# Kernel tuning notes

Hardware: AMD Instinct MI355X
Metric: run time of the kernel (lower is better)

## Reference

```python
import jax, jax.numpy as jnp
import numpy as np

B, S, D, H = 2, 2048, 1024, 16
HD = D // H  # head_dim = 64
NEG = -1.0e9


def setup_inputs() -> dict:
    key = jax.random.key(0)
    ks = jax.random.split(key, 9)
    s = 1.0 / np.sqrt(D)
    return {
        "x": jax.random.normal(ks[0], (B, S, D), jnp.float32),
        "mask": jnp.ones((B, S), jnp.float32),
        "Wq": jax.random.normal(ks[1], (D, D), jnp.float32) * s,
        "bq": jnp.zeros((D,), jnp.float32),
        "Wk": jax.random.normal(ks[2], (D, D), jnp.float32) * s,
        "bk": jnp.zeros((D,), jnp.float32),
        "Wv": jax.random.normal(ks[3], (D, D), jnp.float32) * s,
        "bv": jnp.zeros((D,), jnp.float32),
        "Wo": jax.random.normal(ks[4], (D, D), jnp.float32) * s,
        "bo": jnp.zeros((D,), jnp.float32),
    }


def reference(x, mask, Wq, bq, Wk, bk, Wv, bv, Wo, bo):
    # QKV projections -> [B, H, S, HD]
    def proj(t, W, b):
        return (t @ W + b).reshape(B, S, H, HD).transpose(0, 2, 1, 3)

    q = proj(x, Wq, bq)
    k = proj(x, Wk, bk)
    v = proj(x, Wv, bv)

    scores = jnp.einsum("bhqd,bhkd->bhqk", q, k) / jnp.sqrt(jnp.asarray(HD, x.dtype))
    # causal mask: scores * m + (1-m) * -1e9 (matches original exactly)
    cm = jnp.tril(jnp.ones((S, S), x.dtype))[None, None]
    scores = scores * cm + (1.0 - cm) * NEG
    # 2D padding mask branch
    scores = scores + (1.0 - mask[:, None, None, :]) * NEG

    attn = jax.nn.softmax(scores, axis=-1)
    out = jnp.einsum("bhqk,bhkd->bqhd", attn, v).reshape(B, S, D)
    return out @ Wo + bo
```

## Files before the change

### kernel.cpp

```cpp
#include <hip/hip_runtime.h>
#include <hip/hip_bf16.h>
#include <cstdint>
#include <cstddef>

typedef __attribute__((ext_vector_type(8))) short short8;
typedef __attribute__((ext_vector_type(4))) float floatx4;
typedef __attribute__((ext_vector_type(2))) unsigned int uintx2;

#define MFMA16(a, b, c) __builtin_amdgcn_mfma_f32_16x16x32_bf16((a), (b), (c), 0, 0, 0)
#define LOG2E 1.44269504088896340736f
#define EXP2(x) __builtin_amdgcn_exp2f(x)

__device__ __forceinline__ unsigned short f2bf(float f) {
  unsigned int u = __builtin_bit_cast(unsigned int, f);
  u += 0x7fffu + ((u >> 16) & 1u);
  return (unsigned short)(u >> 16);
}

__device__ __forceinline__ unsigned int pk2(float a, float b) {
  float2 f; f.x = a; f.y = b;
  __hip_bfloat162 h = __float22bfloat162_rn(f);
  unsigned int u;
  __builtin_memcpy(&u, &h, 4);
  return u;
}

typedef __attribute__((address_space(1))) void gvoid_t;
typedef __attribute__((address_space(3))) void svoid_t;
__device__ __forceinline__ void gload_lds16(const void* g, void* l) {
  __builtin_amdgcn_global_load_lds((gvoid_t*)(uintptr_t)g, (svoid_t*)(uintptr_t)l, 16, 0, 0);
}

__global__ void convert_x(const float* __restrict__ x, unsigned short* __restrict__ xb) {
  int i = (blockIdx.x * 256 + threadIdx.x) * 4;
  floatx4 v = *(const floatx4*)(x + i);
  uintx2 o;
  o[0] = pk2(v[0], v[1]);
  o[1] = pk2(v[2], v[3]);
  *(uintx2*)(xb + i) = o;
}

__global__ void transpose_w(const float* __restrict__ Wq, const float* __restrict__ Wk,
                            const float* __restrict__ Wv, const float* __restrict__ Wo,
                            unsigned short* __restrict__ Wqkvt, unsigned short* __restrict__ Wot) {
  __shared__ float tile[32][33];
  int z = blockIdx.z;
  const float* W = (z == 0) ? Wq : (z == 1) ? Wk : (z == 2) ? Wv : Wo;
  unsigned short* out = (z == 3) ? Wot : (Wqkvt + (size_t)z * 1024 * 1024);
  int n0 = blockIdx.x * 32, k0 = blockIdx.y * 32;
  int tx = threadIdx.x, ty = threadIdx.y;
#pragma unroll
  for (int j = 0; j < 4; ++j)
    tile[ty + j * 8][tx] = W[(size_t)(k0 + ty + j * 8) * 1024 + n0 + tx];
  __syncthreads();
#pragma unroll
  for (int j = 0; j < 4; ++j)
    out[(size_t)(n0 + ty + j * 8) * 1024 + k0 + tx] = f2bf(tile[tx][ty + j * 8]);
}

#define GEMM_PROLOGUE()                                                        \
  __shared__ __align__(16) unsigned short As[128 * 64];                        \
  __shared__ __align__(16) unsigned short Bs[128 * 64];                        \
  const int tid = threadIdx.x;                                                 \
  const int lane = tid & 63;                                                   \
  const int wid = tid >> 6;                                                    \
  const int col = lane & 15;                                                   \
  const int quad = lane >> 4;                                                  \
  const int m0 = blockIdx.x * 128;                                             \
  const int n0 = blockIdx.y * 128;                                             \
  const int wm = wid >> 1;                                                     \
  const int wn = wid & 1;                                                      \
  floatx4 acc[4][4];                                                           \
  _Pragma("unroll") for (int i = 0; i < 4; ++i)                                \
      _Pragma("unroll") for (int j = 0; j < 4; ++j)                            \
          acc[i][j] = (floatx4)(0.f);                                          \
  _Pragma("unroll 1") for (int kt = 0; kt < 16; ++kt) {                        \
    __syncthreads();                                                           \
    _Pragma("unroll") for (int call = 0; call < 4; ++call) {                   \
      int c = call * 256 + tid;                                                \
      int r = c >> 3, ch = c & 7;                                              \
      gload_lds16(A + (size_t)(m0 + r) * 1024 + kt * 64 + ((ch ^ (r & 7)) * 8),\
                  As + (size_t)(call * 256 + wid * 64) * 8);                   \
      gload_lds16(Bt + (size_t)(n0 + r) * 1024 + kt * 64 + ((ch ^ (r & 7)) * 8),\
                  Bs + (size_t)(call * 256 + wid * 64) * 8);                   \
    }                                                                          \
    __syncthreads();                                                           \
    _Pragma("unroll") for (int ks = 0; ks < 2; ++ks) {                         \
      short8 af[4], bf[4];                                                     \
      _Pragma("unroll") for (int rt = 0; rt < 4; ++rt) {                       \
        int row = wm * 64 + rt * 16 + col;                                     \
        af[rt] = *(const short8*)&As[row * 64 + (((ks * 4 + quad) ^ (row & 7)) * 8)]; \
      }                                                                        \
      _Pragma("unroll") for (int ct = 0; ct < 4; ++ct) {                       \
        int row = wn * 64 + ct * 16 + col;                                     \
        bf[ct] = *(const short8*)&Bs[row * 64 + (((ks * 4 + quad) ^ (row & 7)) * 8)]; \
      }                                                                        \
      _Pragma("unroll") for (int rt = 0; rt < 4; ++rt)                         \
          _Pragma("unroll") for (int ct = 0; ct < 4; ++ct)                     \
              acc[rt][ct] = MFMA16(af[rt], bf[ct], acc[rt][ct]);               \
    }                                                                          \
  }

__global__ __launch_bounds__(256, 3)
void gemm_qkv(const unsigned short* __restrict__ A, const unsigned short* __restrict__ Bt,
              const float* __restrict__ bq, const float* __restrict__ bk,
              const float* __restrict__ bv,
              unsigned short* __restrict__ Qo, unsigned short* __restrict__ Ko,
              unsigned short* __restrict__ Vo) {
  GEMM_PROLOGUE()
  const int nseg = n0 >> 10;
  const float* bias = (nseg == 0) ? bq : ((nseg == 1) ? bk : bv);
#pragma unroll
  for (int rt = 0; rt < 4; ++rt) {
#pragma unroll
    for (int ct = 0; ct < 4; ++ct) {
      int mg = m0 + wm * 64 + rt * 16 + quad * 4;
      int ng = n0 + wn * 64 + ct * 16 + col;
      int c = ng & 1023;
      int hh = c >> 6, hd = c & 63;
      int b_ = mg >> 11, s = mg & 2047;
      float bb = bias[c];
      if (nseg == 2) {
        uintx2 pk;
        pk[0] = pk2(acc[rt][ct][0] + bb, acc[rt][ct][1] + bb);
        pk[1] = pk2(acc[rt][ct][2] + bb, acc[rt][ct][3] + bb);
        *(uintx2*)&Vo[(size_t)(b_ * 16 + hh) * 131072 + (size_t)hd * 2048 + s] = pk;
      } else {
        unsigned short* dst =
            ((nseg == 0) ? Qo : Ko) + ((size_t)(b_ * 16 + hh) * 2048 + s) * 64 + hd;
        float scl = (nseg == 0) ? (0.125f * LOG2E) : 1.0f;
#pragma unroll
        for (int i = 0; i < 4; ++i) dst[(size_t)i * 64] = f2bf((acc[rt][ct][i] + bb) * scl);
      }
    }
  }
}

__global__ __launch_bounds__(256, 3)
void gemm_out(const unsigned short* __restrict__ A, const unsigned short* __restrict__ Bt,
              const float* __restrict__ bo, float* __restrict__ Out) {
  GEMM_PROLOGUE()
#pragma unroll
  for (int rt = 0; rt < 4; ++rt) {
#pragma unroll
    for (int ct = 0; ct < 4; ++ct) {
      int mg = m0 + wm * 64 + rt * 16 + quad * 4;
      int ng = n0 + wn * 64 + ct * 16 + col;
      float bb = bo[ng];
#pragma unroll
      for (int i = 0; i < 4; ++i)
        Out[(size_t)(mg + i) * 1024 + ng] = acc[rt][ct][i] + bb;
    }
  }
}

__global__ __launch_bounds__(256, 4)
void flash_attn(const unsigned short* __restrict__ Q, const unsigned short* __restrict__ K,
                const unsigned short* __restrict__ Vt, const float* __restrict__ mask,
                unsigned short* __restrict__ O) {
  __shared__ __align__(16) unsigned short Ks[128 * 64];
  __shared__ __align__(16) unsigned short Vs[64 * 128];

  const int tid = threadIdx.x;
  const int lane = tid & 63;
  const int wid = tid >> 6;
  const int col = lane & 15;
  const int quad = lane >> 4;
  const int slot = (int)(blockIdx.x >> 8);
  const int g = (int)(blockIdx.x & 255);
  const int h8 = g >> 5;
  const int bh = g & 31;
  const int j = (slot == 0) ? (31 - h8) : (slot == 1) ? h8 : (slot == 2) ? (23 - h8) : (8 + h8);
  const int b = bh >> 4, h = bh & 15;
  const int q0 = j * 64;
  const int tdiag = j >> 1;

  const unsigned short* Qp = Q + (size_t)bh * 2048 * 64;
  const unsigned short* Kp = K + (size_t)bh * 2048 * 64;
  const unsigned short* Vp = Vt + (size_t)bh * 64 * 2048;
  const float* mp = mask + b * 2048;

  const int lr8 = lane >> 3, lc8 = lane & 7;
  const int lr16 = lane >> 4, lc16 = lane & 15;
  const floatx4 fzero = (floatx4)(0.f);
  const floatx4 fone = (floatx4)(1.f);

#pragma unroll
  for (int i = 0; i < 2; ++i) {
    int seg = wid * 2 + i;
    int r = seg * 8 + lr8;
    gload_lds16(Qp + (size_t)(q0 + r) * 64 + ((lc8 ^ (r & 7)) * 8), Ks + seg * 512);
  }
  __syncthreads();
  short8 qf[2];
  {
    int q = wid * 16 + col;
#pragma unroll
    for (int ks = 0; ks < 2; ++ks)
      qf[ks] = *(const short8*)&Ks[q * 64 + (((ks * 4 + quad) ^ (q & 7)) * 8)];
  }
  unsigned int mbits = 0;
  for (int t = 0; t <= tdiag; ++t) {
    float2 mv = *(const float2*)&mp[t * 128 + lane * 2];
    unsigned long long bb = __ballot(mv.x != 1.f || mv.y != 1.f);
    mbits |= (bb ? 1u : 0u) << t;
  }

  floatx4 o[4];
#pragma unroll
  for (int dt = 0; dt < 4; ++dt) o[dt] = fzero;
  float mrow = -1e30f;
  float lrow = 0.f;

#pragma unroll 1
  for (int t = 0; t <= tdiag; ++t) {
    __syncthreads();
#pragma unroll
    for (int i = 0; i < 4; ++i) {
      int seg = wid * 4 + i;
      int r = seg * 8 + lr8;
      gload_lds16(Kp + (size_t)(t * 128 + r) * 64 + ((lc8 ^ (r & 7)) * 8), Ks + seg * 512);
    }
#pragma unroll
    for (int i = 0; i < 4; ++i) {
      int seg = wid * 4 + i;
      int r = seg * 4 + lr16;
      gload_lds16(Vp + (size_t)r * 2048 + t * 128 + ((lc16 ^ (r & 15)) * 8), Vs + seg * 512);
    }
    __syncthreads();

    floatx4 sc[8];
    __builtin_amdgcn_s_setprio(1);
#pragma unroll
    for (int rt = 0; rt < 8; ++rt) {
      int kr = rt * 16 + col;
      short8 kf0 = *(const short8*)&Ks[kr * 64 + ((quad ^ (col & 7)) * 8)];
      short8 kf1 = *(const short8*)&Ks[kr * 64 + (((4 + quad) ^ (col & 7)) * 8)];
      floatx4 s0 = MFMA16(kf0, qf[0], fzero);
      sc[rt] = MFMA16(kf1, qf[1], s0);
    }
    __builtin_amdgcn_s_setprio(0);
    __syncthreads();

    if (__builtin_amdgcn_readfirstlane(mbits >> t) & 1) {
#pragma unroll
      for (int rt = 0; rt < 8; ++rt) {
        floatx4 mm = *(const floatx4*)&mp[t * 128 + rt * 16 + quad * 4];
        sc[rt] += (fone - mm) * (-1.0e9f * LOG2E);
      }
    }
    if (t == tdiag) {
      int qg = q0 + wid * 16 + col;
#pragma unroll
      for (int rt = 0; rt < 8; ++rt)
#pragma unroll
        for (int i = 0; i < 4; ++i)
          if (t * 128 + rt * 16 + quad * 4 + i > qg) sc[rt][i] = -1.0e9f * LOG2E;
    }

    float mt = -1e30f;
#pragma unroll
    for (int rt = 0; rt < 8; ++rt)
      mt = fmaxf(mt, fmaxf(fmaxf(sc[rt][0], sc[rt][1]), fmaxf(sc[rt][2], sc[rt][3])));
    mt = fmaxf(mt, __shfl_xor(mt, 16));
    mt = fmaxf(mt, __shfl_xor(mt, 32));

    const bool skip = (__all(mt - mrow <= 8.0f) != 0);
    float mn = mrow;
    if (!skip) {
      mn = fmaxf(mrow, mt);
      float alpha = EXP2(mrow - mn);
      mrow = mn;
      lrow *= alpha;
#pragma unroll
      for (int dt = 0; dt < 4; ++dt) o[dt] *= alpha;
    }
    float sum = 0.f;
#pragma unroll
    for (int rt = 0; rt < 8; ++rt)
#pragma unroll
      for (int i = 0; i < 4; ++i) {
        float p = EXP2(sc[rt][i] - mn);
        sc[rt][i] = p;
        sum += p;
      }
    sum += __shfl_xor(sum, 16);
    sum += __shfl_xor(sum, 32);
    lrow += sum;

    {
      int qloc = wid * 16 + col;
#pragma unroll
      for (int rt = 0; rt < 8; ++rt) {
        uintx2 w;
        w[0] = pk2(sc[rt][0], sc[rt][1]);
        w[1] = pk2(sc[rt][2], sc[rt][3]);
        int chunk = (rt * 2 + (quad >> 1)) ^ col;
        *(uintx2*)&Ks[qloc * 128 + chunk * 8 + (quad & 1) * 4] = w;
      }
    }
    __builtin_amdgcn_s_setprio(1);
#pragma unroll
    for (int ks = 0; ks < 4; ++ks) {
      int ch = ks * 4 + quad;
      short8 pf = *(const short8*)&Ks[(wid * 16 + col) * 128 + ((ch ^ col) * 8)];
#pragma unroll
      for (int dt = 0; dt < 4; ++dt) {
        short8 vf = *(const short8*)&Vs[(dt * 16 + col) * 128 + ((ch ^ col) * 8)];
        o[dt] = MFMA16(vf, pf, o[dt]);
      }
    }
    __builtin_amdgcn_s_setprio(0);
  }

  {
    float inv = 1.0f / lrow;
    int qg = q0 + wid * 16 + col;
    unsigned short* dst = O + ((size_t)(b * 2048 + qg)) * 1024 + h * 64;
#pragma unroll
    for (int dt = 0; dt < 4; ++dt) {
      uintx2 pk;
      pk[0] = pk2(o[dt][0] * inv, o[dt][1] * inv);
      pk[1] = pk2(o[dt][2] * inv, o[dt][3] * inv);
      *(uintx2*)&dst[dt * 16 + quad * 4] = pk;
    }
  }
}

extern "C" void kernel_launch(void* const* d_in, const int* in_sizes, int n_in,
                              void* d_out, int out_size, void* d_ws, size_t ws_size,
                              hipStream_t stream) {
  (void)in_sizes; (void)n_in; (void)out_size; (void)ws_size;
  const float* x  = (const float*)d_in[0];
  const float* mask = (const float*)d_in[1];
  const float* Wq = (const float*)d_in[2];
  const float* bq = (const float*)d_in[3];
  const float* Wk = (const float*)d_in[4];
  const float* bk = (const float*)d_in[5];
  const float* Wv = (const float*)d_in[6];
  const float* bv = (const float*)d_in[7];
  const float* Wo = (const float*)d_in[8];
  const float* bo = (const float*)d_in[9];
  float* out = (float*)d_out;

  char* ws = (char*)d_ws;
  unsigned short* xb    = (unsigned short*)(ws);
  unsigned short* Wqkvt = (unsigned short*)(ws + (8u << 20));
  unsigned short* Wot   = (unsigned short*)(ws + (14u << 20));
  unsigned short* Qb    = (unsigned short*)(ws + (16u << 20));
  unsigned short* Kb    = (unsigned short*)(ws + (24u << 20));
  unsigned short* Vtb   = (unsigned short*)(ws + (32u << 20));
  unsigned short* Ao    = (unsigned short*)(ws + (40u << 20));

  convert_x<<<4096, 256, 0, stream>>>(x, xb);
  transpose_w<<<dim3(32, 32, 4), dim3(32, 8), 0, stream>>>(Wq, Wk, Wv, Wo, Wqkvt, Wot);
  gemm_qkv<<<dim3(32, 24), 256, 0, stream>>>(xb, Wqkvt, bq, bk, bv, Qb, Kb, Vtb);
  flash_attn<<<dim3(1024), 256, 0, stream>>>(Qb, Kb, Vtb, mask, Ao);
  gemm_out<<<dim3(32, 8), 256, 0, stream>>>(Ao, Wot, bo, out);
}
```

Baseline: 183.6 us.

## Stage V epilogue through LDS, halve out-GEMM tile, compute row sums via MFMA

The QKV GEMM now writes the transposed V output through shared memory so each thread issues 16-byte contiguous stores instead of scattered 8-byte ones. The output-projection GEMM switches to 64x128 tiles with twice as many blocks and a higher occupancy bound, so more of the GPU's compute units stay busy. In flash attention, the softmax denominator is computed by an MFMA against a vector of bf16 ones instead of scalar adds plus cross-lane shuffles. This sums the rounded bf16 probabilities, which slightly changes numerics, and adds one MFMA per k-step.

```diff
diff --git a/kernel.cpp b/kernel.cpp
--- a/kernel.cpp
+++ b/kernel.cpp
@@ -6,6 +6,7 @@
 typedef __attribute__((ext_vector_type(8))) short short8;
 typedef __attribute__((ext_vector_type(4))) float floatx4;
 typedef __attribute__((ext_vector_type(2))) unsigned int uintx2;
+typedef __attribute__((ext_vector_type(4))) unsigned int uintx4;
 
 #define MFMA16(a, b, c) __builtin_amdgcn_mfma_f32_16x16x32_bf16((a), (b), (c), 0, 0, 0)
 #define LOG2E 1.44269504088896340736f
@@ -58,9 +59,10 @@
     out[(size_t)(n0 + ty + j * 8) * 1024 + k0 + tx] = f2bf(tile[tx][ty + j * 8]);
 }
 
-#define GEMM_PROLOGUE()                                                        \
-  __shared__ __align__(16) unsigned short As[128 * 64];                        \
-  __shared__ __align__(16) unsigned short Bs[128 * 64];                        \
+#define GEMM_PROLOGUE128()                                                     \
+  __shared__ __align__(16) unsigned short Sh[2 * 128 * 64];                    \
+  unsigned short* const As = Sh;                                               \
+  unsigned short* const Bs = Sh + 128 * 64;                                    \
   const int tid = threadIdx.x;                                                 \
   const int lane = tid & 63;                                                   \
   const int wid = tid >> 6;                                                    \
@@ -101,31 +103,107 @@
     }                                                                          \
   }
 
+#define GEMM_PROLOGUE64()                                                      \
+  __shared__ __align__(16) unsigned short As[64 * 64];                         \
+  __shared__ __align__(16) unsigned short Bs[128 * 64];                        \
+  const int tid = threadIdx.x;                                                 \
+  const int lane = tid & 63;                                                   \
+  const int wid = tid >> 6;                                                    \
+  const int col = lane & 15;                                                   \
+  const int quad = lane >> 4;                                                  \
+  const int m0 = blockIdx.x * 64;                                              \
+  const int n0 = blockIdx.y * 128;                                             \
+  const int wm = wid >> 1;                                                     \
+  const int wn = wid & 1;                                                      \
+  floatx4 acc[2][4];                                                           \
+  _Pragma("unroll") for (int i = 0; i < 2; ++i)                                \
+      _Pragma("unroll") for (int j = 0; j < 4; ++j)                            \
+          acc[i][j] = (floatx4)(0.f);                                          \
+  _Pragma("unroll 1") for (int kt = 0; kt < 16; ++kt) {                        \
+    __syncthreads();                                                           \
+    _Pragma("unroll") for (int call = 0; call < 2; ++call) {                   \
+      int c = call * 256 + tid;                                                \
+      int r = c >> 3, ch = c & 7;                                              \
+      gload_lds16(A + (size_t)(m0 + r) * 1024 + kt * 64 + ((ch ^ (r & 7)) * 8),\
+                  As + (size_t)(call * 256 + wid * 64) * 8);                   \
+    }                                                                          \
+    _Pragma("unroll") for (int call = 0; call < 4; ++call) {                   \
+      int c = call * 256 + tid;                                                \
+      int r = c >> 3, ch = c & 7;                                              \
+      gload_lds16(Bt + (size_t)(n0 + r) * 1024 + kt * 64 + ((ch ^ (r & 7)) * 8),\
+                  Bs + (size_t)(call * 256 + wid * 64) * 8);                   \
+    }                                                                          \
+    __syncthreads();                                                           \
+    _Pragma("unroll") for (int ks = 0; ks < 2; ++ks) {                         \
+      short8 af[2], bf[4];                                                     \
+      _Pragma("unroll") for (int rt = 0; rt < 2; ++rt) {                       \
+        int row = wm * 32 + rt * 16 + col;                                     \
+        af[rt] = *(const short8*)&As[row * 64 + (((ks * 4 + quad) ^ (row & 7)) * 8)]; \
+      }                                                                        \
+      _Pragma("unroll") for (int ct = 0; ct < 4; ++ct) {                       \
+        int row = wn * 64 + ct * 16 + col;                                     \
+        bf[ct] = *(const short8*)&Bs[row * 64 + (((ks * 4 + quad) ^ (row & 7)) * 8)]; \
+      }                                                                        \
+      _Pragma("unroll") for (int rt = 0; rt < 2; ++rt)                         \
+          _Pragma("unroll") for (int ct = 0; ct < 4; ++ct)                     \
+              acc[rt][ct] = MFMA16(af[rt], bf[ct], acc[rt][ct]);               \
+    }                                                                          \
+  }
+
 __global__ __launch_bounds__(256, 3)
 void gemm_qkv(const unsigned short* __restrict__ A, const unsigned short* __restrict__ Bt,
               const float* __restrict__ bq, const float* __restrict__ bk,
               const float* __restrict__ bv,
               unsigned short* __restrict__ Qo, unsigned short* __restrict__ Ko,
               unsigned short* __restrict__ Vo) {
-  GEMM_PROLOGUE()
+  GEMM_PROLOGUE128()
   const int nseg = n0 >> 10;
   const float* bias = (nseg == 0) ? bq : ((nseg == 1) ? bk : bv);
-#pragma unroll
-  for (int rt = 0; rt < 4; ++rt) {
-#pragma unroll
-    for (int ct = 0; ct < 4; ++ct) {
-      int mg = m0 + wm * 64 + rt * 16 + quad * 4;
-      int ng = n0 + wn * 64 + ct * 16 + col;
-      int c = ng & 1023;
-      int hh = c >> 6, hd = c & 63;
-      int b_ = mg >> 11, s = mg & 2047;
-      float bb = bias[c];
-      if (nseg == 2) {
-        uintx2 pk;
-        pk[0] = pk2(acc[rt][ct][0] + bb, acc[rt][ct][1] + bb);
-        pk[1] = pk2(acc[rt][ct][2] + bb, acc[rt][ct][3] + bb);
-        *(uintx2*)&Vo[(size_t)(b_ * 16 + hh) * 131072 + (size_t)hd * 2048 + s] = pk;
-      } else {
+  if (nseg == 2) {
+    __syncthreads();
+    const int cb = n0 & 1023;
+#pragma unroll
+    for (int rt = 0; rt < 4; ++rt) {
+#pragma unroll
+      for (int ct = 0; ct < 4; ++ct) {
+        int cl = wn * 64 + ct * 16 + col;
+        int mb = wm * 16 + rt * 4 + quad;
+        float bb = bias[cb + cl];
+        uintx2 w;
+        w[0] = pk2(acc[rt][ct][0] + bb, acc[rt][ct][1] + bb);
+        w[1] = pk2(acc[rt][ct][2] + bb, acc[rt][ct][3] + bb);
+        *(uintx2*)&Sh[cl * 128 + ((mb ^ (cl & 31)) * 4)] = w;
+      }
+    }
+    __syncthreads();
+    {
+      int cl = tid >> 1, half = tid & 1;
+      int hh = (cb >> 6) + (cl >> 6);
+      int hd = cl & 63;
+      int b_ = m0 >> 11;
+      int s0 = (m0 & 2047) + half * 64;
+      unsigned short* dst = Vo + (size_t)(b_ * 16 + hh) * 131072 + (size_t)hd * 2048 + s0;
+#pragma unroll
+      for (int k = 0; k < 8; ++k) {
+        int mb0 = half * 16 + k * 2;
+        uintx2 lo = *(const uintx2*)&Sh[cl * 128 + ((mb0 ^ (cl & 31)) * 4)];
+        uintx2 hi = *(const uintx2*)&Sh[cl * 128 + (((mb0 + 1) ^ (cl & 31)) * 4)];
+        uintx4 v;
+        v[0] = lo[0]; v[1] = lo[1]; v[2] = hi[0]; v[3] = hi[1];
+        *(uintx4*)&dst[k * 8] = v;
+      }
+    }
+  } else {
+#pragma unroll
+    for (int rt = 0; rt < 4; ++rt) {
+#pragma unroll
+      for (int ct = 0; ct < 4; ++ct) {
+        int mg = m0 + wm * 64 + rt * 16 + quad * 4;
+        int ng = n0 + wn * 64 + ct * 16 + col;
+        int c = ng & 1023;
+        int hh = c >> 6, hd = c & 63;
+        int b_ = mg >> 11, s = mg & 2047;
+        float bb = bias[c];
         unsigned short* dst =
             ((nseg == 0) ? Qo : Ko) + ((size_t)(b_ * 16 + hh) * 2048 + s) * 64 + hd;
         float scl = (nseg == 0) ? (0.125f * LOG2E) : 1.0f;
@@ -136,15 +214,15 @@
   }
 }
 
-__global__ __launch_bounds__(256, 3)
+__global__ __launch_bounds__(256, 5)
 void gemm_out(const unsigned short* __restrict__ A, const unsigned short* __restrict__ Bt,
               const float* __restrict__ bo, float* __restrict__ Out) {
-  GEMM_PROLOGUE()
-#pragma unroll
-  for (int rt = 0; rt < 4; ++rt) {
+  GEMM_PROLOGUE64()
+#pragma unroll
+  for (int rt = 0; rt < 2; ++rt) {
 #pragma unroll
     for (int ct = 0; ct < 4; ++ct) {
-      int mg = m0 + wm * 64 + rt * 16 + quad * 4;
+      int mg = m0 + wm * 32 + rt * 16 + quad * 4;
       int ng = n0 + wn * 64 + ct * 16 + col;
       float bb = bo[ng];
 #pragma unroll
@@ -184,6 +262,7 @@
   const int lr16 = lane >> 4, lc16 = lane & 15;
   const floatx4 fzero = (floatx4)(0.f);
   const floatx4 fone = (floatx4)(1.f);
+  const short8 ones8 = (short8)(short)0x3F80;
 
 #pragma unroll
   for (int i = 0; i < 2; ++i) {
@@ -275,18 +354,10 @@
 #pragma unroll
       for (int dt = 0; dt < 4; ++dt) o[dt] *= alpha;
     }
-    float sum = 0.f;
 #pragma unroll
     for (int rt = 0; rt < 8; ++rt)
 #pragma unroll
-      for (int i = 0; i < 4; ++i) {
-        float p = EXP2(sc[rt][i] - mn);
-        sc[rt][i] = p;
-        sum += p;
-      }
-    sum += __shfl_xor(sum, 16);
-    sum += __shfl_xor(sum, 32);
-    lrow += sum;
+      for (int i = 0; i < 4; ++i) sc[rt][i] = EXP2(sc[rt][i] - mn);
 
     {
       int qloc = wid * 16 + col;
@@ -299,11 +370,13 @@
         *(uintx2*)&Ks[qloc * 128 + chunk * 8 + (quad & 1) * 4] = w;
       }
     }
+    floatx4 ssum = fzero;
     __builtin_amdgcn_s_setprio(1);
 #pragma unroll
     for (int ks = 0; ks < 4; ++ks) {
       int ch = ks * 4 + quad;
       short8 pf = *(const short8*)&Ks[(wid * 16 + col) * 128 + ((ch ^ col) * 8)];
+      ssum = MFMA16(ones8, pf, ssum);
 #pragma unroll
       for (int dt = 0; dt < 4; ++dt) {
         short8 vf = *(const short8*)&Vs[(dt * 16 + col) * 128 + ((ch ^ col) * 8)];
@@ -311,6 +384,7 @@
       }
     }
     __builtin_amdgcn_s_setprio(0);
+    lrow += ssum[0];
   }
 
   {
@@ -356,5 +430,5 @@
   transpose_w<<<dim3(32, 32, 4), dim3(32, 8), 0, stream>>>(Wq, Wk, Wv, Wo, Wqkvt, Wot);
   gemm_qkv<<<dim3(32, 24), 256, 0, stream>>>(xb, Wqkvt, bq, bk, bv, Qb, Kb, Vtb);
   flash_attn<<<dim3(1024), 256, 0, stream>>>(Qb, Kb, Vtb, mask, Ao);
-  gemm_out<<<dim3(32, 8), 256, 0, stream>>>(Ao, Wot, bo, out);
-}
+  gemm_out<<<dim3(64, 8), 256, 0, stream>>>(Ao, Wot, bo, out);
+}
```

After: 182.8 us. Within noise of the previous version (-0.5%).
